# Performance work log

Hardware: AMD Instinct MI355X
Metric: run time of the kernel (lower is better)

The kernel has to match this reference:

```python
import jax, jax.numpy as jnp
import numpy as np

N_NODES = 100000


def _gcn_norm(edges, n_nodes):
    # PyG GCNConv: add self-loops, symmetric normalization D^{-1/2}(A+I)D^{-1/2}
    loop = jnp.arange(n_nodes, dtype=edges.dtype)
    src = jnp.concatenate([edges[0], loop])
    dst = jnp.concatenate([edges[1], loop])
    ones = jnp.ones(src.shape[0], dtype=jnp.float32)
    deg = jax.ops.segment_sum(ones, dst, num_segments=n_nodes)  # >=1 thanks to self-loops
    dinv = jax.lax.rsqrt(deg)
    norm = dinv[src] * dinv[dst]  # [E + N]
    return src, dst, norm


def _gcn_conv(x, W, b, src, dst, norm, n_nodes):
    # lin -> gather -> scale -> scatter-add -> +bias (PyG GCNConv order)
    h = x @ W                                   # [N, D_out]
    msg = h[src] * norm[:, None]                # [E+N, D_out]
    agg = jax.ops.segment_sum(msg, dst, num_segments=n_nodes)
    return agg + b


def setup_inputs() -> dict:
    key = jax.random.key(0)
    k_x, k_e, k_w1, k_w2 = jax.random.split(key, 4)
    F_in, D_hid, n_labels, n_edges = 128, 128, 32, 625000
    features = jax.random.normal(k_x, (N_NODES, F_in), dtype=jnp.float32)
    edges = jax.random.randint(k_e, (2, n_edges), 0, N_NODES, dtype=jnp.int64)
    W1 = jax.random.normal(k_w1, (F_in, D_hid), dtype=jnp.float32) / np.sqrt(F_in)
    b1 = jnp.zeros((D_hid,), dtype=jnp.float32)
    W2 = jax.random.normal(k_w2, (D_hid, n_labels), dtype=jnp.float32) / np.sqrt(D_hid)
    b2 = jnp.zeros((n_labels,), dtype=jnp.float32)
    return {"features": features, "edges": edges, "W1": W1, "b1": b1, "W2": W2, "b2": b2}


def reference(features, edges, W1, b1, W2, b2):
    n_nodes = features.shape[0]
    src, dst, norm = _gcn_norm(edges, n_nodes)
    h1 = jax.nn.relu(_gcn_conv(features, W1, b1, src, dst, norm, n_nodes))
    h2 = _gcn_conv(h1, W2, b2, src, dst, norm, n_nodes)
    return jax.nn.log_softmax(h2, axis=1)
```

## Files before the change

### kernel.cpp

```cpp
#include <hip/hip_runtime.h>

#define NN 100000
#define MAXDEG 64

typedef _Float16 f16;
typedef f16 f16x2 __attribute__((ext_vector_type(2)));
typedef f16 f16x8 __attribute__((ext_vector_type(8)));
typedef float f32x4 __attribute__((ext_vector_type(4)));

__device__ __forceinline__ int detect_is64(const void* edges, int E) {
    const long long* p = (const long long*)edges;
    int m = E < 1024 ? E : 1024;
    int bad = 0;
    for (int i = (threadIdx.x & 63); i < m; i += 64) {
        if ((unsigned long long)p[i] >= (unsigned long long)NN) bad = 1;
    }
    return !__any(bad);
}

__device__ __forceinline__ int edge_at(const void* e, long i, int is64) {
    return is64 ? (int)((const long long*)e)[i] : ((const int*)e)[i];
}

__global__ __launch_bounds__(256) void k_prep(const float* __restrict__ W1,
                                              const float* __restrict__ W2,
                                              f16* __restrict__ BT1,
                                              f16* __restrict__ BT2,
                                              int* __restrict__ deg, int n) {
    int t = blockIdx.x * blockDim.x + threadIdx.x;
    int stride = gridDim.x * blockDim.x;
    for (int i = t; i < n; i += stride) deg[i] = 0;
    for (int i = t; i < 128 * 128; i += stride) {
        int nn = i >> 7, kk = i & 127;
        BT1[i] = (f16)W1[kk * 128 + nn];
    }
    for (int i = t; i < 32 * 128; i += stride) {
        int nn = i >> 7, kk = i & 127;
        BT2[i] = (f16)W2[kk * 32 + nn];
    }
}

__global__ __launch_bounds__(256) void k_geb(const float* __restrict__ X,
                                             const f16* __restrict__ BT,
                                             f16* __restrict__ H, int n,
                                             const void* edges, int E,
                                             int* __restrict__ deg,
                                             int* __restrict__ csr,
                                             int nG, int nF) {
    __shared__ __align__(16) unsigned char Bs[16384];
    const int bid = blockIdx.x;
    const int lo = nG < nF ? nG : nF;
    int gid = -1, fid = -1;
    if (bid < 2 * lo) {
        if ((bid & 1) == 0) gid = bid >> 1; else fid = bid >> 1;
    } else if (nG > nF) {
        gid = bid - lo;
    } else {
        fid = bid - lo;
    }

    if (fid >= 0) {
        int is64 = detect_is64(edges, E);
        long stride = (long)nF * 256;
        for (long e = (long)fid * 256 + threadIdx.x; e < E; e += stride) {
            int s = edge_at(edges, e, is64);
            int d = edge_at(edges, (long)E + e, is64);
            int t = atomicAdd(&deg[d], 1);
            if (t < MAXDEG) csr[(long)d * MAXDEG + t] = s;
        }
        return;
    }

    const int tid = threadIdx.x;
    const int wave = tid >> 6;
    const int lane = tid & 63;
    const int lrow = lane & 15;
    const int kgrp = lane >> 4;
    const int row0 = gid * 64 + wave * 16;
    int arow = row0 + lrow;
    if (arow >= n) arow = n - 1;

    f16x8 a[4];
#pragma unroll
    for (int ks = 0; ks < 4; ks++) {
        const float* ap = &X[(long)arow * 128 + ks * 32 + kgrp * 8];
        float4 v0 = *(const float4*)ap;
        float4 v1 = *(const float4*)(ap + 4);
        f16x8 tv;
        tv[0] = (f16)v0.x; tv[1] = (f16)v0.y; tv[2] = (f16)v0.z; tv[3] = (f16)v0.w;
        tv[4] = (f16)v1.x; tv[5] = (f16)v1.y; tv[6] = (f16)v1.z; tv[7] = (f16)v1.w;
        a[ks] = tv;
    }

    const int sw = (lrow & 7) << 4;
#pragma unroll
    for (int half = 0; half < 2; half++) {
#pragma unroll
        for (int s = 0; s < 4; s++) {
            int L = (tid + s * 256) * 16;
            int row = L >> 8;
            f16x8 v = *(const f16x8*)((const unsigned char*)BT + half * 16384 + L);
            *(f16x8*)(Bs + (L ^ ((row & 7) << 4))) = v;
        }
        __syncthreads();
#pragma unroll
        for (int ntl = 0; ntl < 4; ntl++) {
            f32x4 acc = {0.f, 0.f, 0.f, 0.f};
            const int bbase = (ntl * 16 + lrow) * 256 + kgrp * 16;
#pragma unroll
            for (int ks = 0; ks < 4; ks++) {
                f16x8 b = *(const f16x8*)(Bs + ((bbase + ks * 64) ^ sw));
                acc = __builtin_amdgcn_mfma_f32_16x16x32_f16(a[ks], b, acc, 0, 0, 0);
            }
            const int col = (half * 4 + ntl) * 16 + lrow;
#pragma unroll
            for (int r = 0; r < 4; r++) {
                int grow = row0 + kgrp * 4 + r;
                if (grow < n) H[(long)grow * 128 + col] = (f16)acc[r];
            }
        }
        __syncthreads();
    }
}

__global__ __launch_bounds__(256) void k_gemm2(const f16* __restrict__ A,
                                               const f16* __restrict__ BT,
                                               f16* __restrict__ H, int n) {
    __shared__ __align__(16) unsigned char Bs[8192];
    const int tid = threadIdx.x;
    {
        int L = tid * 16;
        int row = L >> 8;
        f16x8 v = *(const f16x8*)((const unsigned char*)BT + L);
        *(f16x8*)(Bs + (L ^ ((row & 7) << 4))) = v;
        L += 4096; row = L >> 8;
        v = *(const f16x8*)((const unsigned char*)BT + L);
        *(f16x8*)(Bs + (L ^ ((row & 7) << 4))) = v;
    }
    __syncthreads();

    const int wave = tid >> 6;
    const int lane = tid & 63;
    const int lrow = lane & 15;
    const int kgrp = lane >> 4;
    const int row0 = blockIdx.x * 64 + wave * 16;
    if (row0 >= n) return;
    int arow = row0 + lrow;
    if (arow >= n) arow = n - 1;

    f16x8 a[4];
#pragma unroll
    for (int ks = 0; ks < 4; ks++)
        a[ks] = *(const f16x8*)&A[(long)arow * 128 + ks * 32 + kgrp * 8];

    const int sw = (lrow & 7) << 4;
#pragma unroll
    for (int nt = 0; nt < 2; nt++) {
        f32x4 acc = {0.f, 0.f, 0.f, 0.f};
        const int bbase = (nt * 16 + lrow) * 256 + kgrp * 16;
#pragma unroll
        for (int ks = 0; ks < 4; ks++) {
            f16x8 b = *(const f16x8*)(Bs + ((bbase + ks * 64) ^ sw));
            acc = __builtin_amdgcn_mfma_f32_16x16x32_f16(a[ks], b, acc, 0, 0, 0);
        }
        const int col = nt * 16 + lrow;
#pragma unroll
        for (int r = 0; r < 4; r++) {
            int grow = row0 + kgrp * 4 + r;
            if (grow < n) H[(long)grow * 32 + col] = (f16)acc[r];
        }
    }
}

__global__ __launch_bounds__(256) void k_spmm1(const f16* __restrict__ H,
                                               const int* __restrict__ deg,
                                               const int* __restrict__ csr,
                                               const float* __restrict__ b1,
                                               f16* __restrict__ O, int n) {
    const int lane = threadIdx.x & 15;
    const int nhw = (gridDim.x * blockDim.x) >> 4;
    const f16x8* H8 = (const f16x8*)H;
    const float4 bl = *(const float4*)&b1[lane * 8];
    const float4 bh = *(const float4*)&b1[lane * 8 + 4];
    for (int node = (blockIdx.x * blockDim.x + threadIdx.x) >> 4; node < n;
         node += nhw) {
        int dg = deg[node];
        float di = rsqrtf((float)(dg + 1));
        float w0 = di * di;
        f16x8 self = H8[(long)node * 16 + lane];
        float acc0[8], acc1[8], acc2[8], acc3[8];
#pragma unroll
        for (int j = 0; j < 8; j++) {
            acc0[j] = w0 * (float)self[j];
            acc1[j] = 0.f; acc2[j] = 0.f; acc3[j] = 0.f;
        }
        int s0 = node * MAXDEG;
        int s1 = s0 + (dg < MAXDEG ? dg : MAXDEG);
        int i = s0;
        for (; i + 4 <= s1; i += 4) {
            int sA = csr[i], sB = csr[i + 1], sC = csr[i + 2], sD = csr[i + 3];
            f16x8 vA = H8[(long)sA * 16 + lane];
            f16x8 vB = H8[(long)sB * 16 + lane];
            f16x8 vC = H8[(long)sC * 16 + lane];
            f16x8 vD = H8[(long)sD * 16 + lane];
            float wA = rsqrtf((float)(deg[sA] + 1)) * di;
            float wB = rsqrtf((float)(deg[sB] + 1)) * di;
            float wC = rsqrtf((float)(deg[sC] + 1)) * di;
            float wD = rsqrtf((float)(deg[sD] + 1)) * di;
#pragma unroll
            for (int j = 0; j < 8; j++) {
                acc0[j] += wA * (float)vA[j];
                acc1[j] += wB * (float)vB[j];
                acc2[j] += wC * (float)vC[j];
                acc3[j] += wD * (float)vD[j];
            }
        }
        for (; i < s1; i++) {
            int s = csr[i];
            float w = rsqrtf((float)(deg[s] + 1)) * di;
            f16x8 v = H8[(long)s * 16 + lane];
#pragma unroll
            for (int j = 0; j < 8; j++) acc0[j] += w * (float)v[j];
        }
        f16x8 o;
        o[0] = (f16)fmaxf(acc0[0] + acc1[0] + acc2[0] + acc3[0] + bl.x, 0.f);
        o[1] = (f16)fmaxf(acc0[1] + acc1[1] + acc2[1] + acc3[1] + bl.y, 0.f);
        o[2] = (f16)fmaxf(acc0[2] + acc1[2] + acc2[2] + acc3[2] + bl.z, 0.f);
        o[3] = (f16)fmaxf(acc0[3] + acc1[3] + acc2[3] + acc3[3] + bl.w, 0.f);
        o[4] = (f16)fmaxf(acc0[4] + acc1[4] + acc2[4] + acc3[4] + bh.x, 0.f);
        o[5] = (f16)fmaxf(acc0[5] + acc1[5] + acc2[5] + acc3[5] + bh.y, 0.f);
        o[6] = (f16)fmaxf(acc0[6] + acc1[6] + acc2[6] + acc3[6] + bh.z, 0.f);
        o[7] = (f16)fmaxf(acc0[7] + acc1[7] + acc2[7] + acc3[7] + bh.w, 0.f);
        ((f16x8*)O)[(long)node * 16 + lane] = o;
    }
}

__global__ __launch_bounds__(256) void k_spmm2(const f16* __restrict__ H,
                                               const int* __restrict__ deg,
                                               const int* __restrict__ csr,
                                               const float* __restrict__ b2,
                                               float* __restrict__ out, int n) {
    const int lane = threadIdx.x & 15;
    const int stot = (gridDim.x * blockDim.x) >> 4;
    const f16x2* H2 = (const f16x2*)H;
    const float2 bias = *(const float2*)&b2[lane * 2];
    for (int node = (blockIdx.x * blockDim.x + threadIdx.x) >> 4; node < n;
         node += stot) {
        int dg = deg[node];
        float di = rsqrtf((float)(dg + 1));
        float w0 = di * di;
        f16x2 self = H2[(long)node * 16 + lane];
        float a0 = w0 * (float)self[0], a1 = w0 * (float)self[1];
        float b0 = 0.f, b1v = 0.f, c0 = 0.f, c1 = 0.f, d0 = 0.f, d1 = 0.f;
        int s0 = node * MAXDEG;
        int s1 = s0 + (dg < MAXDEG ? dg : MAXDEG);
        int i = s0;
        for (; i + 4 <= s1; i += 4) {
            int sA = csr[i], sB = csr[i + 1], sC = csr[i + 2], sD = csr[i + 3];
            f16x2 vA = H2[(long)sA * 16 + lane];
            f16x2 vB = H2[(long)sB * 16 + lane];
            f16x2 vC = H2[(long)sC * 16 + lane];
            f16x2 vD = H2[(long)sD * 16 + lane];
            float wA = rsqrtf((float)(deg[sA] + 1)) * di;
            float wB = rsqrtf((float)(deg[sB] + 1)) * di;
            float wC = rsqrtf((float)(deg[sC] + 1)) * di;
            float wD = rsqrtf((float)(deg[sD] + 1)) * di;
            a0 += wA * (float)vA[0]; a1 += wA * (float)vA[1];
            b0 += wB * (float)vB[0]; b1v += wB * (float)vB[1];
            c0 += wC * (float)vC[0]; c1 += wC * (float)vC[1];
            d0 += wD * (float)vD[0]; d1 += wD * (float)vD[1];
        }
        for (; i < s1; i++) {
            int s = csr[i];
            float w = rsqrtf((float)(deg[s] + 1)) * di;
            f16x2 v = H2[(long)s * 16 + lane];
            a0 += w * (float)v[0]; a1 += w * (float)v[1];
        }
        float acc0 = a0 + b0 + c0 + d0 + bias.x;
        float acc1 = a1 + b1v + c1 + d1 + bias.y;
        float m = fmaxf(acc0, acc1);
#pragma unroll
        for (int off = 8; off >= 1; off >>= 1) m = fmaxf(m, __shfl_xor(m, off));
        float l = expf(acc0 - m) + expf(acc1 - m);
#pragma unroll
        for (int off = 8; off >= 1; off >>= 1) l += __shfl_xor(l, off);
        float lg = m + logf(l);
        *(float2*)&out[(long)node * 32 + lane * 2] =
            make_float2(acc0 - lg, acc1 - lg);
    }
}

extern "C" void kernel_launch(void* const* d_in, const int* in_sizes, int n_in,
                              void* d_out, int out_size, void* d_ws, size_t ws_size,
                              hipStream_t stream) {
    const float* X  = (const float*)d_in[0];
    const void* edges = d_in[1];
    const float* W1 = (const float*)d_in[2];
    const float* b1 = (const float*)d_in[3];
    const float* W2 = (const float*)d_in[4];
    const float* b2 = (const float*)d_in[5];
    float* out = (float*)d_out;

    const int n = in_sizes[0] / 128;
    const int E = in_sizes[1] / 2;

    char* w = (char*)d_ws;
    auto alloc = [&](size_t bytes) -> char* {
        char* p = w;
        w += (bytes + 511) & ~(size_t)511;
        return p;
    };
    int* deg = (int*)alloc((size_t)n * 4);
    int* csr = (int*)alloc((size_t)n * MAXDEG * 4);
    f16* BT1 = (f16*)alloc(128 * 128 * 2);
    f16* BT2 = (f16*)alloc(32 * 128 * 2);
    f16* h1  = (f16*)alloc((size_t)n * 128 * 2);
    f16* h1b = (f16*)alloc((size_t)n * 128 * 2);
    f16* h2  = (f16*)alloc((size_t)n * 32 * 2);

    k_prep<<<256, 256, 0, stream>>>(W1, W2, BT1, BT2, deg, n);

    const int nG = (n + 63) / 64;
    const int nF = 2048;
    k_geb<<<nG + nF, 256, 0, stream>>>(X, BT1, h1, n, edges, E, deg, csr, nG, nF);

    k_spmm1<<<2048, 256, 0, stream>>>(h1, deg, csr, b1, h1b, n);
    k_gemm2<<<(n + 63) / 64, 256, 0, stream>>>(h1b, BT2, h2, n);
    k_spmm2<<<2048, 256, 0, stream>>>(h2, deg, csr, b2, out, n);
}
```

Before: 112.7 us.

## Split fused GEMM/edge-binning kernel into separate bin and gemm1 launches

Breaks apart the fused kernel, which interleaved GEMM blocks with edge-binning blocks so they could overlap. Edge binning now runs as its own kernel, followed by a standalone GEMM kernel. The change also issues the deg[] loads in the SpMM loops before the H gathers, and doubles the prep grid. This loses the overlap between the atomic binning and the compute-heavy GEMM and adds one launch, in exchange for simpler kernels that may each schedule better.

```diff
diff --git a/kernel.cpp b/kernel.cpp
--- a/kernel.cpp
+++ b/kernel.cpp
@@ -40,43 +40,28 @@
     }
 }
 
-__global__ __launch_bounds__(256) void k_geb(const float* __restrict__ X,
-                                             const f16* __restrict__ BT,
-                                             f16* __restrict__ H, int n,
-                                             const void* edges, int E,
-                                             int* __restrict__ deg,
-                                             int* __restrict__ csr,
-                                             int nG, int nF) {
+__global__ void k_bin(const void* edges, int E, int* __restrict__ deg,
+                      int* __restrict__ csr) {
+    int is64 = detect_is64(edges, E);
+    for (long e = blockIdx.x * (long)blockDim.x + threadIdx.x; e < E;
+         e += (long)gridDim.x * blockDim.x) {
+        int s = edge_at(edges, e, is64);
+        int d = edge_at(edges, (long)E + e, is64);
+        int t = atomicAdd(&deg[d], 1);
+        if (t < MAXDEG) csr[(long)d * MAXDEG + t] = s;
+    }
+}
+
+__global__ __launch_bounds__(256) void k_gemm1(const float* __restrict__ X,
+                                               const f16* __restrict__ BT,
+                                               f16* __restrict__ H, int n) {
     __shared__ __align__(16) unsigned char Bs[16384];
-    const int bid = blockIdx.x;
-    const int lo = nG < nF ? nG : nF;
-    int gid = -1, fid = -1;
-    if (bid < 2 * lo) {
-        if ((bid & 1) == 0) gid = bid >> 1; else fid = bid >> 1;
-    } else if (nG > nF) {
-        gid = bid - lo;
-    } else {
-        fid = bid - lo;
-    }
-
-    if (fid >= 0) {
-        int is64 = detect_is64(edges, E);
-        long stride = (long)nF * 256;
-        for (long e = (long)fid * 256 + threadIdx.x; e < E; e += stride) {
-            int s = edge_at(edges, e, is64);
-            int d = edge_at(edges, (long)E + e, is64);
-            int t = atomicAdd(&deg[d], 1);
-            if (t < MAXDEG) csr[(long)d * MAXDEG + t] = s;
-        }
-        return;
-    }
-
     const int tid = threadIdx.x;
     const int wave = tid >> 6;
     const int lane = tid & 63;
     const int lrow = lane & 15;
     const int kgrp = lane >> 4;
-    const int row0 = gid * 64 + wave * 16;
+    const int row0 = blockIdx.x * 64 + wave * 16;
     int arow = row0 + lrow;
     if (arow >= n) arow = n - 1;
 
@@ -199,14 +184,15 @@
         int i = s0;
         for (; i + 4 <= s1; i += 4) {
             int sA = csr[i], sB = csr[i + 1], sC = csr[i + 2], sD = csr[i + 3];
+            int dA = deg[sA], dB = deg[sB], dC = deg[sC], dD = deg[sD];
             f16x8 vA = H8[(long)sA * 16 + lane];
             f16x8 vB = H8[(long)sB * 16 + lane];
             f16x8 vC = H8[(long)sC * 16 + lane];
             f16x8 vD = H8[(long)sD * 16 + lane];
-            float wA = rsqrtf((float)(deg[sA] + 1)) * di;
-            float wB = rsqrtf((float)(deg[sB] + 1)) * di;
-            float wC = rsqrtf((float)(deg[sC] + 1)) * di;
-            float wD = rsqrtf((float)(deg[sD] + 1)) * di;
+            float wA = rsqrtf((float)(dA + 1)) * di;
+            float wB = rsqrtf((float)(dB + 1)) * di;
+            float wC = rsqrtf((float)(dC + 1)) * di;
+            float wD = rsqrtf((float)(dD + 1)) * di;
 #pragma unroll
             for (int j = 0; j < 8; j++) {
                 acc0[j] += wA * (float)vA[j];
@@ -257,14 +243,15 @@
         int i = s0;
         for (; i + 4 <= s1; i += 4) {
             int sA = csr[i], sB = csr[i + 1], sC = csr[i + 2], sD = csr[i + 3];
+            int dA = deg[sA], dB = deg[sB], dC = deg[sC], dD = deg[sD];
             f16x2 vA = H2[(long)sA * 16 + lane];
             f16x2 vB = H2[(long)sB * 16 + lane];
             f16x2 vC = H2[(long)sC * 16 + lane];
             f16x2 vD = H2[(long)sD * 16 + lane];
-            float wA = rsqrtf((float)(deg[sA] + 1)) * di;
-            float wB = rsqrtf((float)(deg[sB] + 1)) * di;
-            float wC = rsqrtf((float)(deg[sC] + 1)) * di;
-            float wD = rsqrtf((float)(deg[sD] + 1)) * di;
+            float wA = rsqrtf((float)(dA + 1)) * di;
+            float wB = rsqrtf((float)(dB + 1)) * di;
+            float wC = rsqrtf((float)(dC + 1)) * di;
+            float wD = rsqrtf((float)(dD + 1)) * di;
             a0 += wA * (float)vA[0]; a1 += wA * (float)vA[1];
             b0 += wB * (float)vB[0]; b1v += wB * (float)vB[1];
             c0 += wC * (float)vC[0]; c1 += wC * (float)vC[1];
@@ -318,13 +305,12 @@
     f16* h1b = (f16*)alloc((size_t)n * 128 * 2);
     f16* h2  = (f16*)alloc((size_t)n * 32 * 2);
 
-    k_prep<<<256, 256, 0, stream>>>(W1, W2, BT1, BT2, deg, n);
-
-    const int nG = (n + 63) / 64;
-    const int nF = 2048;
-    k_geb<<<nG + nF, 256, 0, stream>>>(X, BT1, h1, n, edges, E, deg, csr, nG, nF);
-
+    k_prep<<<512, 256, 0, stream>>>(W1, W2, BT1, BT2, deg, n);
+    k_bin<<<2048, 256, 0, stream>>>(edges, E, deg, csr);
+
+    const int gb = (n + 63) / 64;
+    k_gemm1<<<gb, 256, 0, stream>>>(X, BT1, h1, n);
     k_spmm1<<<2048, 256, 0, stream>>>(h1, deg, csr, b1, h1b, n);
-    k_gemm2<<<(n + 63) / 64, 256, 0, stream>>>(h1b, BT2, h2, n);
+    k_gemm2<<<gb, 256, 0, stream>>>(h1b, BT2, h2, n);
     k_spmm2<<<2048, 256, 0, stream>>>(h2, deg, csr, b2, out, n);
 }
```

Result: slower. 130.4 us (+15.8%).
